# Performance work log

Hardware: AMD Instinct MI355X
Metric: run time of the kernel (lower is better)

The kernel has to match this reference:

```python
import jax, jax.numpy as jnp
import numpy as np

DT_MIN, DT_MAX = 1e-3, 0.1
DT_RANK, D_STATE, D_CONV = 64, 16, 4


def setup_inputs() -> dict:
    key = jax.random.key(0)
    ks = jax.random.split(key, 8)
    B, T, Dm = 4, 4096, 1024
    Dn = 2 * Dm  # expand * d_model
    s = lambda k, shape, scale=0.02: (jax.random.normal(k, shape, jnp.float32) * scale)
    return {
        "x": jax.random.normal(ks[0], (B, T, Dm), jnp.float32),
        "W_in": s(ks[1], (2 * Dn, Dm)),
        "conv_w": s(ks[2], (Dn, 1, D_CONV), 0.1),
        "conv_b": jnp.zeros((Dn,), jnp.float32),
        "W_x": s(ks[3], (DT_RANK + 2 * D_STATE, Dn)),
        "W_dt": s(ks[4], (Dn, DT_RANK)),
        "b_dt": jnp.zeros((Dn,), jnp.float32),
        "log_A": jax.random.uniform(ks[5], (Dn, D_STATE), jnp.float32),
        "D_param": jnp.ones((Dn,), jnp.float32),
        "W_out": s(ks[6], (Dm, Dn)),
        "ln_w": jnp.ones((Dm,), jnp.float32),
        "ln_b": jnp.zeros((Dm,), jnp.float32),
    }


def reference(x, W_in, conv_w, conv_b, W_x, W_dt, b_dt, log_A, D_param, W_out, ln_w, ln_b):
    B, T, Dm = x.shape
    Dn = W_dt.shape[0]
    residual = x
    # LayerNorm (biased variance, eps=1e-5, as torch)
    mu = x.mean(-1, keepdims=True)
    var = x.var(-1, keepdims=True)
    xn = (x - mu) / jnp.sqrt(var + 1e-5) * ln_w + ln_b
    # in_proj -> split into x_inner, z
    xz = xn @ W_in.T  # (B,T,2*Dn)
    x_inner, z = jnp.split(xz, 2, axis=-1)
    # causal depthwise conv (torch pads both sides d_conv-1 then slices [:T] == left-pad only)
    xc = jnp.transpose(x_inner, (0, 2, 1))  # (B,Dn,T)
    xc = jax.lax.conv_general_dilated(
        xc, conv_w, window_strides=(1,), padding=[(D_CONV - 1, 0)],
        dimension_numbers=("NCH", "OIH", "NCH"), feature_group_count=Dn)
    xc = xc + conv_b[None, :, None]
    u = jax.nn.silu(jnp.transpose(xc, (0, 2, 1)))  # (B,T,Dn)
    # input-dependent dt, B, C
    xbc = u @ W_x.T
    dt_low, B_ssm, C_ssm = jnp.split(xbc, [DT_RANK, DT_RANK + D_STATE], axis=-1)
    dt = jax.nn.softplus(dt_low @ W_dt.T + b_dt) + DT_MIN
    dt = jnp.clip(dt, DT_MIN, DT_MAX)  # (B,T,Dn)
    A = -jnp.exp(log_A)  # (Dn,N), always negative -> stable
    # selective scan: h_t = exp(dt*A)*h_{t-1} + (dt*u)*B_t ; y_t = <C_t, h_t>
    def step(h, inp):
        dt_t, u_t, B_t, C_t = inp  # (B,Dn),(B,Dn),(B,N),(B,N)
        dA = jnp.exp(dt_t[:, :, None] * A)  # (B,Dn,N)
        h = dA * h + (dt_t * u_t)[:, :, None] * B_t[:, None, :]
        y = jnp.einsum("bdn,bn->bd", h, C_t)
        return h, y

    h0 = jnp.zeros((B, Dn, D_STATE), x.dtype)
    _, ys = jax.lax.scan(
        step, h0,
        (jnp.moveaxis(dt, 1, 0), jnp.moveaxis(u, 1, 0),
         jnp.moveaxis(B_ssm, 1, 0), jnp.moveaxis(C_ssm, 1, 0)))
    y = jnp.moveaxis(ys, 0, 1)  # (B,T,Dn)
    y = y + u * D_param
    y = y * jax.nn.silu(z)
    return y @ W_out.T + residual
```

## Files before the change

kernel.cpp:

```cpp
#include <hip/hip_runtime.h>
#include <cstdint>
#include <cstddef>

#define TT 4096
#define DM 1024
#define DN 2048
#define MROWS 16384
#define NCH 64
#define CHL 64
#define SW 16
#define XBCS 128

typedef unsigned short u16;
typedef u16 ushort8_t __attribute__((ext_vector_type(8)));
typedef u16 ushort4_t __attribute__((ext_vector_type(4)));
typedef short bf16x8 __attribute__((ext_vector_type(8)));
typedef float f32x4 __attribute__((ext_vector_type(4)));

#define EXP2(x) __builtin_amdgcn_exp2f(x)
#define L2E 1.44269504f

__device__ __forceinline__ float bf2f(u16 b) {
  return __uint_as_float(((unsigned int)b) << 16);
}
__device__ __forceinline__ u16 f2bf(float f) {
  unsigned int u = __float_as_uint(f);
  u = u + 0x7FFFu + ((u >> 16) & 1u);
  return (u16)(u >> 16);
}
__device__ __forceinline__ u16 f2h(float f) {
  _Float16 h = (_Float16)f;
  return __builtin_bit_cast(u16, h);
}
__device__ __forceinline__ float h2f(u16 v) {
  return (float)__builtin_bit_cast(_Float16, v);
}

__device__ __forceinline__ void gload_lds16(const void* g, void* l) {
  __builtin_amdgcn_global_load_lds(
      (const __attribute__((address_space(1))) unsigned int*)g,
      (__attribute__((address_space(3))) unsigned int*)l, 16, 0, 0);
}

#define FENCE() asm volatile("" ::: "memory")

__global__ __launch_bounds__(256) void cvt_bf16_kernel(const float* __restrict__ in,
    u16* __restrict__ out, int n4) {
  int i = blockIdx.x * 256 + threadIdx.x;
  if (i >= n4) return;
  float4 v = ((const float4*)in)[i];
  ushort4_t o; o[0] = f2bf(v.x); o[1] = f2bf(v.y); o[2] = f2bf(v.z); o[3] = f2bf(v.w);
  ((ushort4_t*)out)[i] = o;
}

__global__ __launch_bounds__(256) void cvt_wx_kernel(const float* __restrict__ W_x,
    u16* __restrict__ out) {
  int i = blockIdx.x * 256 + threadIdx.x;
  int row = i >> 9;
  ushort4_t o;
  if (row < 96) {
    float4 v = ((const float4*)W_x)[i];
    o[0] = f2bf(v.x); o[1] = f2bf(v.y); o[2] = f2bf(v.z); o[3] = f2bf(v.w);
  } else {
    o[0] = 0; o[1] = 0; o[2] = 0; o[3] = 0;
  }
  ((ushort4_t*)out)[i] = o;
}

__global__ __launch_bounds__(256) void ln_kernel(const float* __restrict__ x,
    const float* __restrict__ ln_w, const float* __restrict__ ln_b,
    u16* __restrict__ xn) {
  int row = blockIdx.x;
  int tid = threadIdx.x;
  const float4* xr = (const float4*)(x + (size_t)row * DM);
  float4 v = xr[tid];
  float s  = v.x + v.y + v.z + v.w;
  float s2 = v.x*v.x + v.y*v.y + v.z*v.z + v.w*v.w;
#pragma unroll
  for (int o = 32; o > 0; o >>= 1) { s += __shfl_down(s, o, 64); s2 += __shfl_down(s2, o, 64); }
  __shared__ float red[2][4];
  __shared__ float mv[2];
  int wid = tid >> 6, lane = tid & 63;
  if (lane == 0) { red[0][wid] = s; red[1][wid] = s2; }
  __syncthreads();
  if (tid == 0) {
    float a  = red[0][0] + red[0][1] + red[0][2] + red[0][3];
    float b2 = red[1][0] + red[1][1] + red[1][2] + red[1][3];
    float mean = a * (1.f / DM);
    float var  = b2 * (1.f / DM) - mean * mean;
    mv[0] = mean; mv[1] = rsqrtf(var + 1e-5f);
  }
  __syncthreads();
  float mean = mv[0], inv = mv[1];
  float4 w = ((const float4*)ln_w)[tid];
  float4 b = ((const float4*)ln_b)[tid];
  ushort4_t o;
  o[0] = f2bf((v.x - mean) * inv * w.x + b.x);
  o[1] = f2bf((v.y - mean) * inv * w.y + b.y);
  o[2] = f2bf((v.z - mean) * inv * w.z + b.z);
  o[3] = f2bf((v.w - mean) * inv * w.w + b.w);
  *(ushort4_t*)(xn + (size_t)row * DM + tid * 4) = o;
}

template<int MODE>
__global__ __launch_bounds__(256) void gemm_mfma_nt(
    const u16* __restrict__ A, int lda,
    const u16* __restrict__ B, int ldb,
    void* __restrict__ Cp, int ldc,
    const float* __restrict__ Res, int K,
    const float* __restrict__ bias, u16* __restrict__ dl_out) {
  __shared__ __align__(16) u16 a_s[128 * 64];
  __shared__ __align__(16) u16 b_s[128 * 64];
  const int tid = threadIdx.x;
  const int w = tid >> 6, l = tid & 63;
  const int wr = w >> 1, wc = w & 1;
  const int nbx = gridDim.x, gy = gridDim.y;
  int lin = blockIdx.y * nbx + blockIdx.x;
  int xcd = lin & 7;
  int m = lin >> 3;
  int bi, bj;
  if (gy >= 8) {
    int njx = gy >> 3;
    bi = m / njx;
    bj = xcd * njx + m % njx;
  } else {
    int cpx = (nbx * gy) >> 3;
    int swz = xcd * cpx + m;
    bi = swz % nbx; bj = swz / nbx;
  }
  const int lrow = l >> 3;
  const int scol = ((l & 7) ^ lrow) * 16;

  f32x4 acc[4][4] = {};

  const u16* Abase = A + (size_t)(bi * 128 + w * 8 + lrow) * lda;
  const u16* Bbase = B + (size_t)(bj * 128 + w * 8 + lrow) * ldb;

  for (int k0 = 0; k0 < K; k0 += 64) {
#pragma unroll
    for (int c = 0; c < 4; c++) {
      const char* ga = (const char*)(Abase + (size_t)(c * 32) * lda + k0) + scol;
      const char* gb = (const char*)(Bbase + (size_t)(c * 32) * ldb + k0) + scol;
      gload_lds16(ga, (char*)a_s + c * 4096 + w * 1024);
      gload_lds16(gb, (char*)b_s + c * 4096 + w * 1024);
    }
    __syncthreads();
#pragma unroll
    for (int kk = 0; kk < 2; kk++) {
      bf16x8 af[4], bfr[4];
#pragma unroll
      for (int m2 = 0; m2 < 4; m2++) {
        int fr = wr * 64 + m2 * 16 + (l & 15);
        int cb = (kk * 64 + ((l >> 4) << 4)) ^ ((fr & 7) << 4);
        af[m2] = *(const bf16x8*)((const char*)a_s + fr * 128 + cb);
      }
#pragma unroll
      for (int n = 0; n < 4; n++) {
        int fr = wc * 64 + n * 16 + (l & 15);
        int cb = (kk * 64 + ((l >> 4) << 4)) ^ ((fr & 7) << 4);
        bfr[n] = *(const bf16x8*)((const char*)b_s + fr * 128 + cb);
      }
#pragma unroll
      for (int m2 = 0; m2 < 4; m2++)
#pragma unroll
        for (int n = 0; n < 4; n++)
          acc[m2][n] = __builtin_amdgcn_mfma_f32_16x16x32_bf16(af[m2], bfr[n], acc[m2][n], 0, 0, 0);
    }
    __syncthreads();
  }
  const int col0 = bj * 128 + wc * 64 + (l & 15);
  const int row0 = bi * 128 + wr * 64 + (l >> 4) * 4;
#pragma unroll
  for (int m2 = 0; m2 < 4; m2++)
#pragma unroll
    for (int n = 0; n < 4; n++) {
      int col = col0 + n * 16;
      float bv = 0.f;
      if constexpr (MODE == 3) bv = bias[col];
#pragma unroll
      for (int r = 0; r < 4; r++) {
        size_t row = (size_t)(row0 + m2 * 16 + r);
        float v = acc[m2][n][r];
        if constexpr (MODE == 0) {
          ((u16*)Cp)[row * ldc + col] = f2bf(v);
        } else if constexpr (MODE == 1) {
          ((float*)Cp)[row * ldc + col] = v;
          if (col < 64) dl_out[row * 64 + col] = f2bf(v);
        } else if constexpr (MODE == 2) {
          v += Res[row * ldc + col];
          ((float*)Cp)[row * ldc + col] = v;
        } else {
          float s = v + bv;
          float sp = __logf(1.f + __expf(s));
          float dtv = fminf(sp + 1e-3f, 0.1f);
          ((u16*)Cp)[row * ldc + col] = f2h(dtv);
        }
      }
    }
}

template<int MODE>
__global__ __launch_bounds__(512) void gemm256(
    const u16* __restrict__ A, int lda,
    const u16* __restrict__ B, int ldb,
    void* __restrict__ Cp, int ldc,
    const float* __restrict__ Res, int K) {
  extern __shared__ char smem[];
  const int tid = threadIdx.x;
  const int w = tid >> 6, l = tid & 63;
  const int wm = w >> 2, wn = w & 3;
  const int nbx = gridDim.x, gy = gridDim.y;
  int lin = blockIdx.y * nbx + blockIdx.x;
  int xcd = lin & 7, mm = lin >> 3;
  int bi, bj;
  if (gy >= 8) { int njx = gy >> 3; bi = mm / njx; bj = xcd * njx + mm % njx; }
  else { int cpx = (nbx * gy) >> 3; int swz = xcd * cpx + mm; bi = swz % nbx; bj = swz / nbx; }
  const int lrow = l >> 3;
  const int scol = ((l & 7) ^ lrow) * 16;
  const int l15 = l & 15, lhi = (l >> 4) << 4;
  const u16* aRow = A + (size_t)(bi * 256 + w * 8 + lrow) * lda;
  const u16* bRow = B + (size_t)(bj * 256 + w * 8 + lrow) * ldb;
  char* As = smem;
  char* Bs = smem + 65536;

#define IS_A(s, k) gload_lds16((const char*)(aRow + (size_t)((k) * 64) * lda + (size_t)(s) * 64) + scol, \
                               As + ((((s) & 1)) << 15) + (k) * 8192 + w * 1024)
#define IS_B(s, k) gload_lds16((const char*)(bRow + (size_t)((k) * 64) * ldb + (size_t)(s) * 64) + scol, \
                               Bs + ((((s) & 1)) << 15) + (k) * 8192 + w * 1024)

  f32x4 acc[8][4] = {};
  bf16x8 bf[2][4];
  const int NT = K >> 6;

  IS_B(0, 0); IS_B(0, 1); IS_B(0, 2); IS_B(0, 3);
  IS_A(0, 0); IS_A(0, 2); IS_A(0, 1); IS_A(0, 3);
  IS_B(1, 0); IS_B(1, 1); IS_B(1, 2); IS_B(1, 3); IS_A(1, 0);

#define MFMA8(MLO, KK) do { \
    bf16x8 a0_ = ardA(MLO, KK), a1_ = ardA((MLO) + 1, KK); \
    __builtin_amdgcn_s_setprio(1); \
    _Pragma("unroll") \
    for (int n_ = 0; n_ < 4; n_++) { \
      acc[MLO][n_]       = __builtin_amdgcn_mfma_f32_16x16x32_bf16(a0_, bf[KK][n_], acc[MLO][n_], 0, 0, 0); \
      acc[(MLO) + 1][n_] = __builtin_amdgcn_mfma_f32_16x16x32_bf16(a1_, bf[KK][n_], acc[(MLO) + 1][n_], 0, 0, 0); \
    } \
    __builtin_amdgcn_s_setprio(0); \
  } while (0)

  for (int t = 0; t < NT; ++t) {
    const char* Ab = As + ((t & 1) << 15);
    const char* Bb = Bs + ((t & 1) << 15);
    auto ardA = [&](int m, int kk) {
      int fr = wm * 128 + m * 16 + l15;
      int cb = (kk * 64 + lhi) ^ ((fr & 7) << 4);
      return *(const bf16x8*)(Ab + fr * 128 + cb);
    };
    auto ardB = [&](int n, int kk) {
      int fr = wn * 64 + n * 16 + l15;
      int cb = (kk * 64 + lhi) ^ ((fr & 7) << 4);
      return *(const bf16x8*)(Bb + fr * 128 + cb);
    };
    if (t + 1 < NT) IS_A(t + 1, 2);
    FENCE();
    asm volatile("s_waitcnt vmcnt(8)" ::: "memory");
    __builtin_amdgcn_s_barrier();
    FENCE();
    bf[0][0] = ardB(0, 0); bf[0][1] = ardB(1, 0); bf[0][2] = ardB(2, 0); bf[0][3] = ardB(3, 0);
    MFMA8(0, 0);
    if (t + 1 < NT) IS_A(t + 1, 1);
    MFMA8(2, 0);
    if (t + 1 < NT) IS_A(t + 1, 3);
    bf[1][0] = ardB(0, 1); bf[1][1] = ardB(1, 1); bf[1][2] = ardB(2, 1); bf[1][3] = ardB(3, 1);
    MFMA8(0, 1);
    FENCE();
    __builtin_amdgcn_s_barrier();
    FENCE();
    if (t + 2 < NT) IS_B(t + 2, 0);
    MFMA8(2, 1);
    if (t + 2 < NT) IS_B(t + 2, 1);
    FENCE();
    asm volatile("s_waitcnt vmcnt(10)" ::: "memory");
    __builtin_amdgcn_s_barrier();
    FENCE();
    MFMA8(4, 0);
    if (t + 2 < NT) IS_B(t + 2, 2);
    MFMA8(6, 0);
    if (t + 2 < NT) IS_B(t + 2, 3);
    MFMA8(4, 1);
    if (t + 2 < NT) IS_A(t + 2, 0);
    MFMA8(6, 1);
  }
#undef MFMA8
#undef IS_A
#undef IS_B

  const int col0 = bj * 256 + wn * 64 + l15;
  const int row0 = bi * 256 + wm * 128 + (l >> 4) * 4;
#pragma unroll
  for (int m = 0; m < 8; m++)
#pragma unroll
    for (int n = 0; n < 4; n++) {
      int col = col0 + n * 16;
#pragma unroll
      for (int r = 0; r < 4; r++) {
        size_t row = (size_t)(row0 + m * 16 + r);
        float v = acc[m][n][r];
        if constexpr (MODE == 0) {
          ((u16*)Cp)[row * ldc + col] = f2bf(v);
        } else {
          v += Res[row * ldc + col];
          ((float*)Cp)[row * ldc + col] = v;
        }
      }
    }
}

__global__ __launch_bounds__(256) void conv_silu_kernel(const u16* __restrict__ xz,
    const float* __restrict__ conv_w, const float* __restrict__ conv_b,
    u16* __restrict__ u) {
  size_t gid = (size_t)blockIdx.x * 256 + threadIdx.x;
  int c = (int)(gid & 255);
  size_t i = gid >> 8;
  int t = (int)(i & (TT - 1));
  int d0 = c * 8;
  const u16* base = xz + i * 4096 + d0;
  ushort8_t r0 = *(const ushort8_t*)base;
  ushort8_t r1 = 0, r2 = 0, r3 = 0;
  if (t >= 1) r1 = *(const ushort8_t*)(base - 4096);
  if (t >= 2) r2 = *(const ushort8_t*)(base - 2 * 4096);
  if (t >= 3) r3 = *(const ushort8_t*)(base - 3 * 4096);
  float cbv[8];
  *(float4*)&cbv[0] = *(const float4*)(conv_b + d0);
  *(float4*)&cbv[4] = *(const float4*)(conv_b + d0 + 4);
  ushort8_t o;
#pragma unroll
  for (int j = 0; j < 8; j++) {
    float4 w = *(const float4*)(conv_w + (size_t)(d0 + j) * 4);
    float a = cbv[j] + w.w * bf2f(r0[j]) + w.z * bf2f(r1[j])
            + w.y * bf2f(r2[j]) + w.x * bf2f(r3[j]);
    a = a * __builtin_amdgcn_rcpf(1.f + EXP2(-a * L2E));
    o[j] = f2bf(a);
  }
  *(ushort8_t*)(u + i * 2048 + d0) = o;
}

__global__ __launch_bounds__(256) void scan_part1(u16* u_g,
    const u16* __restrict__ dt_g, const float* __restrict__ xbc,
    const float* __restrict__ log_A, const float* __restrict__ D_param,
    float* __restrict__ hbuf, float* __restrict__ Sbuf) {
  int d0 = blockIdx.x * 128;
  int c  = blockIdx.y;
  int b  = blockIdx.z;
  int tid = threadIdx.x;
  int w = tid >> 6, l = tid & 63;
  int dl = tid >> 1, q = tid & 1, q8 = q << 3;
  int d = d0 + dl;
  __shared__ __align__(16) u16 u_s[2][SW][128];
  __shared__ __align__(16) u16 dts[2][SW][128];
  __shared__ __align__(16) float bc_s[2][SW][32];

  float A2[8];
  {
    float4 la0 = *(const float4*)(log_A + (size_t)d * 16 + q8);
    float4 la1 = *(const float4*)(log_A + (size_t)d * 16 + q8 + 4);
    A2[0] = -EXP2(la0.x * L2E) * L2E; A2[1] = -EXP2(la0.y * L2E) * L2E;
    A2[2] = -EXP2(la0.z * L2E) * L2E; A2[3] = -EXP2(la0.w * L2E) * L2E;
    A2[4] = -EXP2(la1.x * L2E) * L2E; A2[5] = -EXP2(la1.y * L2E) * L2E;
    A2[6] = -EXP2(la1.z * L2E) * L2E; A2[7] = -EXP2(la1.w * L2E) * L2E;
  }
  float Dp = D_param[d];
  float h[8] = {};
  float sdt = 0.f;
  size_t t0 = (size_t)b * TT + (size_t)c * CHL;
  const int sr = w * 4 + (l >> 4);
  const int sc = (l & 15) * 8;
  u16* up = u_g + t0 * 2048 + d;

#define P1STAGE(wnd, pb) { size_t i0_ = t0 + (size_t)(wnd) * SW;                          \
    gload_lds16(u_g  + (i0_ + sr) * 2048 + d0 + sc, (char*)u_s[pb] + w * 1024);           \
    gload_lds16(dt_g + (i0_ + sr) * 4096 + d0 + sc, (char*)dts[pb] + w * 1024);           \
    if (w < 2) gload_lds16(xbc + (i0_ + w * 8 + (l >> 3)) * XBCS + 64 + (l & 7) * 4,      \
                           (char*)bc_s[pb] + w * 1024); }

  P1STAGE(0, 0);
  for (int wnd = 0; wnd < CHL / SW; wnd++) {
    int pb = wnd & 1;
    __syncthreads();
    if (wnd + 1 < CHL / SW) P1STAGE(wnd + 1, pb ^ 1);
#pragma unroll 4
    for (int tt = 0; tt < SW; tt++) {
      float dtv = h2f(dts[pb][tt][dl]);
      float uv  = bf2f(u_s[pb][tt][dl]);
      sdt += dtv;
      float xin = dtv * uv;
      float yv = q ? 0.f : uv * Dp;
      float4 B0 = *(const float4*)&bc_s[pb][tt][q8];
      float4 B1 = *(const float4*)&bc_s[pb][tt][q8 + 4];
      float4 C0 = *(const float4*)&bc_s[pb][tt][16 + q8];
      float4 C1 = *(const float4*)&bc_s[pb][tt][16 + q8 + 4];
      h[0] = __builtin_fmaf(EXP2(dtv * A2[0]), h[0], xin * B0.x); yv = __builtin_fmaf(h[0], C0.x, yv);
      h[1] = __builtin_fmaf(EXP2(dtv * A2[1]), h[1], xin * B0.y); yv = __builtin_fmaf(h[1], C0.y, yv);
      h[2] = __builtin_fmaf(EXP2(dtv * A2[2]), h[2], xin * B0.z); yv = __builtin_fmaf(h[2], C0.z, yv);
      h[3] = __builtin_fmaf(EXP2(dtv * A2[3]), h[3], xin * B0.w); yv = __builtin_fmaf(h[3], C0.w, yv);
      h[4] = __builtin_fmaf(EXP2(dtv * A2[4]), h[4], xin * B1.x); yv = __builtin_fmaf(h[4], C1.x, yv);
      h[5] = __builtin_fmaf(EXP2(dtv * A2[5]), h[5], xin * B1.y); yv = __builtin_fmaf(h[5], C1.y, yv);
      h[6] = __builtin_fmaf(EXP2(dtv * A2[6]), h[6], xin * B1.z); yv = __builtin_fmaf(h[6], C1.z, yv);
      h[7] = __builtin_fmaf(EXP2(dtv * A2[7]), h[7], xin * B1.w); yv = __builtin_fmaf(h[7], C1.w, yv);
      yv += __shfl_xor(yv, 1, 64);
      if (q == 0) *up = f2h(yv);
      up += 2048;
    }
  }
  float* hp = hbuf + (((size_t)b * NCH + c) * 16 + q8) * DN + d;
#pragma unroll
  for (int k = 0; k < 8; k++) hp[(size_t)k * DN] = h[k];
  if (q == 0) Sbuf[((size_t)b * NCH + c) * DN + d] = sdt;
#undef P1STAGE
}

__global__ __launch_bounds__(256) void scan_combine(const float* __restrict__ log_A,
    const float* __restrict__ Sbuf, float* __restrict__ hbuf) {
  int idx = blockIdx.x * 256 + threadIdx.x;
  int dd = idx & (DN - 1), n = (idx >> 11) & 15, b = idx >> 15;
  float A2 = -EXP2(log_A[(size_t)dd * 16 + n] * L2E) * L2E;
  float h = 0.f;
#pragma unroll
  for (int c = 0; c < NCH; c++) {
    size_t off = (((size_t)b * NCH + c) * 16 + n) * DN + dd;
    float hl = hbuf[off];
    float P = EXP2(A2 * Sbuf[((size_t)b * NCH + c) * DN + dd]);
    hbuf[off] = h;
    h = hl + P * h;
  }
}

__global__ __launch_bounds__(256) void scan_part2(u16* yl,
    const u16* __restrict__ xz, const float* __restrict__ xbc,
    const u16* __restrict__ dt_g, const float* __restrict__ log_A,
    const float* __restrict__ hbuf) {
  int d0 = blockIdx.x * 128;
  int c  = blockIdx.y;
  int b  = blockIdx.z;
  int tid = threadIdx.x;
  int w = tid >> 6, l = tid & 63;
  int dl = tid >> 1, q = tid & 1, q8 = q << 3;
  int d = d0 + dl;
  __shared__ __align__(16) u16 yls[2][SW][128];
  __shared__ __align__(16) u16 z_s[2][SW][128];
  __shared__ __align__(16) u16 dts[2][SW][128];
  __shared__ __align__(16) float c_s[2][SW][16];

  float A2[8];
  {
    float4 la0 = *(const float4*)(log_A + (size_t)d * 16 + q8);
    float4 la1 = *(const float4*)(log_A + (size_t)d * 16 + q8 + 4);
    A2[0] = -EXP2(la0.x * L2E) * L2E; A2[1] = -EXP2(la0.y * L2E) * L2E;
    A2[2] = -EXP2(la0.z * L2E) * L2E; A2[3] = -EXP2(la0.w * L2E) * L2E;
    A2[4] = -EXP2(la1.x * L2E) * L2E; A2[5] = -EXP2(la1.y * L2E) * L2E;
    A2[6] = -EXP2(la1.z * L2E) * L2E; A2[7] = -EXP2(la1.w * L2E) * L2E;
  }
  float hs[8];
  {
    const float* hp = hbuf + (((size_t)b * NCH + c) * 16 + q8) * DN + d;
#pragma unroll
    for (int k = 0; k < 8; k++) hs[k] = hp[(size_t)k * DN];
  }
  float cum = 0.f;
  size_t t0 = (size_t)b * TT + (size_t)c * CHL;
  const int sr = w * 4 + (l >> 4);
  const int sc = (l & 15) * 8;
  u16* ylp = yl + t0 * 2048 + d;

#define P2STAGE(wnd, pb) { size_t i0_ = t0 + (size_t)(wnd) * SW;                          \
    gload_lds16(yl   + (i0_ + sr) * 2048 + d0 + sc, (char*)yls[pb] + w * 1024);           \
    gload_lds16(xz   + (i0_ + sr) * 4096 + 2048 + d0 + sc, (char*)z_s[pb] + w * 1024);    \
    gload_lds16(dt_g + (i0_ + sr) * 4096 + d0 + sc, (char*)dts[pb] + w * 1024);           \
    if (w == 0) gload_lds16(xbc + (i0_ + (l >> 2)) * XBCS + 80 + (l & 3) * 4,             \
                            (char*)c_s[pb]); }

  P2STAGE(0, 0);
  for (int wnd = 0; wnd < CHL / SW; wnd++) {
    int pb = wnd & 1;
    __syncthreads();
    if (wnd + 1 < CHL / SW) P2STAGE(wnd + 1, pb ^ 1);
#pragma unroll 4
    for (int tt = 0; tt < SW; tt++) {
      float dtv = h2f(dts[pb][tt][dl]);
      cum += dtv;
      float4 C0 = *(const float4*)&c_s[pb][tt][q8];
      float4 C1 = *(const float4*)&c_s[pb][tt][q8 + 4];
      float yv = C0.x * (EXP2(cum * A2[0]) * hs[0]) + C0.y * (EXP2(cum * A2[1]) * hs[1])
               + C0.z * (EXP2(cum * A2[2]) * hs[2]) + C0.w * (EXP2(cum * A2[3]) * hs[3])
               + C1.x * (EXP2(cum * A2[4]) * hs[4]) + C1.y * (EXP2(cum * A2[5]) * hs[5])
               + C1.z * (EXP2(cum * A2[6]) * hs[6]) + C1.w * (EXP2(cum * A2[7]) * hs[7]);
      if (q == 0) yv += h2f(yls[pb][tt][dl]);
      yv += __shfl_xor(yv, 1, 64);
      float zv = bf2f(z_s[pb][tt][dl]);
      float sig = __builtin_amdgcn_rcpf(1.f + EXP2(-zv * L2E));
      if (q == 0) *ylp = f2bf(yv * zv * sig);
      ylp += 2048;
    }
  }
#undef P2STAGE
}

extern "C" void kernel_launch(void* const* d_in, const int* in_sizes, int n_in,
                              void* d_out, int out_size, void* d_ws, size_t ws_size,
                              hipStream_t stream) {
  const float* x       = (const float*)d_in[0];
  const float* W_in    = (const float*)d_in[1];
  const float* conv_w  = (const float*)d_in[2];
  const float* conv_b  = (const float*)d_in[3];
  const float* W_x     = (const float*)d_in[4];
  const float* W_dt    = (const float*)d_in[5];
  const float* b_dt    = (const float*)d_in[6];
  const float* log_A   = (const float*)d_in[7];
  const float* D_param = (const float*)d_in[8];
  const float* W_out   = (const float*)d_in[9];
  const float* ln_w    = (const float*)d_in[10];
  const float* ln_b    = (const float*)d_in[11];
  float* out = (float*)d_out;

  size_t need = (size_t)MROWS * 4096 * 2 + (size_t)MROWS * DN * 2 + (size_t)MROWS * 96 * 4;
  if (ws_size < need) return;
  u16*   xz  = (u16*)d_ws;
  u16*   u   = xz + (size_t)MROWS * 4096;
  u16*   W_out_b = (u16*)(u + (size_t)MROWS * DN);

  u16*   xn_b    = (u16*)d_out;
  float* xbc     = (float*)d_out;
  float* hbuf    = (float*)((char*)d_out + (8u << 20));
  u16*   W_in_b  = (u16*)((char*)d_out + (40u << 20));
  float* Sbuf    = (float*)((char*)d_out + (48u << 20));
  u16*   W_x_b   = (u16*)((char*)d_out + (50u << 20));
  u16*   W_dt_b  = (u16*)((char*)d_out + (50u << 20) + (512u << 10));
  u16*   dl_b    = (u16*)((char*)d_out + (51u << 20));

  static int use256 = -1;
  if (use256 < 0) {
    hipError_t e0 = hipFuncSetAttribute(reinterpret_cast<const void*>(&gemm256<0>),
        hipFuncAttributeMaxDynamicSharedMemorySize, 131072);
    hipError_t e2 = hipFuncSetAttribute(reinterpret_cast<const void*>(&gemm256<2>),
        hipFuncAttributeMaxDynamicSharedMemorySize, 131072);
    use256 = (e0 == hipSuccess && e2 == hipSuccess) ? 1 : 0;
  }

  cvt_wx_kernel<<<(128 * 2048 / 4) / 256, 256, 0, stream>>>(W_x, W_x_b);
  cvt_bf16_kernel<<<(2048 * 64 / 4) / 256, 256, 0, stream>>>(W_dt, W_dt_b, 2048 * 64 / 4);
  ln_kernel<<<MROWS, 256, 0, stream>>>(x, ln_w, ln_b, xn_b);
  cvt_bf16_kernel<<<(4096 * 1024 / 4) / 256, 256, 0, stream>>>(W_in, W_in_b, 4096 * 1024 / 4);
  if (use256) {
    gemm256<0><<<dim3(MROWS / 256, 4096 / 256), 512, 131072, stream>>>(
        xn_b, DM, W_in_b, DM, xz, 4096, nullptr, DM);
  } else {
    gemm_mfma_nt<0><<<dim3(MROWS / 128, 4096 / 128), 256, 0, stream>>>(
        xn_b, DM, W_in_b, DM, xz, 4096, nullptr, DM, nullptr, nullptr);
  }
  conv_silu_kernel<<<MROWS, 256, 0, stream>>>(xz, conv_w, conv_b, u);
  gemm_mfma_nt<1><<<dim3(MROWS / 128, XBCS / 128), 256, 0, stream>>>(
      u, DN, W_x_b, DN, xbc, XBCS, nullptr, DN, nullptr, dl_b);
  gemm_mfma_nt<3><<<dim3(MROWS / 128, DN / 128), 256, 0, stream>>>(
      dl_b, 64, W_dt_b, 64, xz, 4096, nullptr, 64, b_dt, nullptr);
  scan_part1<<<dim3(DN / 128, NCH, 4), 256, 0, stream>>>(
      u, xz, xbc, log_A, D_param, hbuf, Sbuf);
  scan_combine<<<4 * DN * 16 / 256, 256, 0, stream>>>(log_A, Sbuf, hbuf);
  scan_part2<<<dim3(DN / 128, NCH, 4), 256, 0, stream>>>(
      u, xz, xbc, xz, log_A, hbuf);
  cvt_bf16_kernel<<<(1024 * 2048 / 4) / 256, 256, 0, stream>>>(W_out, W_out_b, 1024 * 2048 / 4);
  if (use256) {
    gemm256<2><<<dim3(MROWS / 256, 1024 / 256), 512, 131072, stream>>>(
        u, DN, W_out_b, DN, out, DM, x, DN);
  } else {
    gemm_mfma_nt<2><<<dim3(MROWS / 128, 1024 / 128), 256, 0, stream>>>(
        u, DN, W_out_b, DN, out, DM, x, DN, nullptr, nullptr);
  }
}
```

Measured before the change: 623.5 us.

## Restructure GEMM main loop into 4 barrier-separated 16-MFMA clusters with one-stage prefetch

Replaces the two-stage-ahead GEMM pipeline, which interleaved 8-MFMA groups with loads, with a one-tile-ahead schedule. Each k-step is split into four phases: read A/B fragments from LDS, issue part of the next tile's global-to-LDS loads, then run a 16-MFMA cluster at raised priority. The goal is to group MFMAs more densely and make LDS reads and prefetch issue more regular. The cost is many more barriers per iteration and a shorter prefetch distance, which can expose global load latency.

After: 619.9 us. About the same (-0.6%).

```diff
diff --git a/kernel.cpp b/kernel.cpp
--- a/kernel.cpp
+++ b/kernel.cpp
@@ -229,21 +229,19 @@
                                Bs + ((((s) & 1)) << 15) + (k) * 8192 + w * 1024)
 
   f32x4 acc[8][4] = {};
-  bf16x8 bf[2][4];
   const int NT = K >> 6;
 
   IS_B(0, 0); IS_B(0, 1); IS_B(0, 2); IS_B(0, 3);
   IS_A(0, 0); IS_A(0, 2); IS_A(0, 1); IS_A(0, 3);
-  IS_B(1, 0); IS_B(1, 1); IS_B(1, 2); IS_B(1, 3); IS_A(1, 0);
-
-#define MFMA8(MLO, KK) do { \
-    bf16x8 a0_ = ardA(MLO, KK), a1_ = ardA((MLO) + 1, KK); \
+
+#define CLUSTER16(AARR, BARR, MBASE) do { \
     __builtin_amdgcn_s_setprio(1); \
     _Pragma("unroll") \
-    for (int n_ = 0; n_ < 4; n_++) { \
-      acc[MLO][n_]       = __builtin_amdgcn_mfma_f32_16x16x32_bf16(a0_, bf[KK][n_], acc[MLO][n_], 0, 0, 0); \
-      acc[(MLO) + 1][n_] = __builtin_amdgcn_mfma_f32_16x16x32_bf16(a1_, bf[KK][n_], acc[(MLO) + 1][n_], 0, 0, 0); \
-    } \
+    for (int m_ = 0; m_ < 4; m_++) \
+      _Pragma("unroll") \
+      for (int n_ = 0; n_ < 4; n_++) \
+        acc[(MBASE) + m_][n_] = __builtin_amdgcn_mfma_f32_16x16x32_bf16( \
+            AARR[m_], BARR[n_], acc[(MBASE) + m_][n_], 0, 0, 0); \
     __builtin_amdgcn_s_setprio(0); \
   } while (0)
 
@@ -260,37 +258,51 @@
       int cb = (kk * 64 + lhi) ^ ((fr & 7) << 4);
       return *(const bf16x8*)(Bb + fr * 128 + cb);
     };
-    if (t + 1 < NT) IS_A(t + 1, 2);
-    FENCE();
-    asm volatile("s_waitcnt vmcnt(8)" ::: "memory");
-    __builtin_amdgcn_s_barrier();
-    FENCE();
-    bf[0][0] = ardB(0, 0); bf[0][1] = ardB(1, 0); bf[0][2] = ardB(2, 0); bf[0][3] = ardB(3, 0);
-    MFMA8(0, 0);
-    if (t + 1 < NT) IS_A(t + 1, 1);
-    MFMA8(2, 0);
-    if (t + 1 < NT) IS_A(t + 1, 3);
-    bf[1][0] = ardB(0, 1); bf[1][1] = ardB(1, 1); bf[1][2] = ardB(2, 1); bf[1][3] = ardB(3, 1);
-    MFMA8(0, 1);
-    FENCE();
-    __builtin_amdgcn_s_barrier();
-    FENCE();
-    if (t + 2 < NT) IS_B(t + 2, 0);
-    MFMA8(2, 1);
-    if (t + 2 < NT) IS_B(t + 2, 1);
-    FENCE();
-    asm volatile("s_waitcnt vmcnt(10)" ::: "memory");
-    __builtin_amdgcn_s_barrier();
-    FENCE();
-    MFMA8(4, 0);
-    if (t + 2 < NT) IS_B(t + 2, 2);
-    MFMA8(6, 0);
-    if (t + 2 < NT) IS_B(t + 2, 3);
-    MFMA8(4, 1);
-    if (t + 2 < NT) IS_A(t + 2, 0);
-    MFMA8(6, 1);
-  }
-#undef MFMA8
+    bf16x8 a[4], b0[4], b1[4];
+    if (t + 1 < NT) {
+      IS_B(t + 1, 0); IS_B(t + 1, 1);
+      FENCE();
+      asm volatile("s_waitcnt vmcnt(2)" ::: "memory");
+    } else {
+      asm volatile("s_waitcnt vmcnt(0)" ::: "memory");
+    }
+    __builtin_amdgcn_s_barrier();
+    FENCE();
+    b0[0] = ardB(0, 0); b0[1] = ardB(1, 0); b0[2] = ardB(2, 0); b0[3] = ardB(3, 0);
+    a[0] = ardA(0, 0); a[1] = ardA(1, 0); a[2] = ardA(2, 0); a[3] = ardA(3, 0);
+    FENCE();
+    if (t + 1 < NT) { IS_B(t + 1, 2); IS_B(t + 1, 3); FENCE(); }
+    __builtin_amdgcn_s_barrier();
+    CLUSTER16(a, b0, 0);
+    FENCE();
+    __builtin_amdgcn_s_barrier();
+    FENCE();
+    a[0] = ardA(4, 0); a[1] = ardA(5, 0); a[2] = ardA(6, 0); a[3] = ardA(7, 0);
+    FENCE();
+    if (t + 1 < NT) { IS_A(t + 1, 0); IS_A(t + 1, 2); FENCE(); }
+    __builtin_amdgcn_s_barrier();
+    CLUSTER16(a, b0, 4);
+    FENCE();
+    __builtin_amdgcn_s_barrier();
+    FENCE();
+    b1[0] = ardB(0, 1); b1[1] = ardB(1, 1); b1[2] = ardB(2, 1); b1[3] = ardB(3, 1);
+    a[0] = ardA(0, 1); a[1] = ardA(1, 1); a[2] = ardA(2, 1); a[3] = ardA(3, 1);
+    FENCE();
+    if (t + 1 < NT) { IS_A(t + 1, 1); IS_A(t + 1, 3); FENCE(); }
+    __builtin_amdgcn_s_barrier();
+    CLUSTER16(a, b1, 0);
+    FENCE();
+    __builtin_amdgcn_s_barrier();
+    FENCE();
+    a[0] = ardA(4, 1); a[1] = ardA(5, 1); a[2] = ardA(6, 1); a[3] = ardA(7, 1);
+    FENCE();
+    __builtin_amdgcn_s_barrier();
+    CLUSTER16(a, b1, 4);
+    FENCE();
+    __builtin_amdgcn_s_barrier();
+    FENCE();
+  }
+#undef CLUSTER16
 #undef IS_A
 #undef IS_B
 
```
